# Kernel tuning notes

Hardware: AMD Instinct MI355X
Metric: run time of the kernel (lower is better)

## Reference

```python
import jax, jax.numpy as jnp
import numpy as np

SCALE = 4.0  # InputEmbedding scale


def setup_inputs() -> dict:
    key = jax.random.key(0)
    ks = jax.random.split(key, 16)
    T_obs, T_pred, N, E, H = 9, 12, 16384, 64, 128
    n_scenes = 512  # N / 32 tracks per scene
    inp = {
        "observed": jax.random.normal(ks[0], (T_obs, N, 2), jnp.float32),
        "prediction": jax.random.normal(ks[1], (T_pred, N, 2), jnp.float32),
        "goals": jax.random.normal(ks[2], (N, 2), jnp.float32),
        "batch_split": jnp.arange(0, N + 1, N // n_scenes, dtype=jnp.int64),
        # InputEmbedding: Linear(2 -> E)
        "W_emb": jax.random.normal(ks[3], (E, 2), jnp.float32) * 0.5,
        "b_emb": jax.random.normal(ks[4], (E,), jnp.float32) * 0.1,
        # LSTMCell(E -> H)
        "W_ih": jax.random.normal(ks[5], (4 * H, E), jnp.float32) * 0.08,
        "W_hh": jax.random.normal(ks[6], (4 * H, H), jnp.float32) * 0.08,
        "b_ih": jax.random.normal(ks[7], (4 * H,), jnp.float32) * 0.05,
        "b_hh": jax.random.normal(ks[8], (4 * H,), jnp.float32) * 0.05,
        # real_classifier MLP: [H, H/2, H/4, 1], ReLU after every Linear
        "W1": jax.random.normal(ks[9], (H // 2, H), jnp.float32) * 0.08,
        "b1": jnp.zeros((H // 2,), jnp.float32),
        "W2": jax.random.normal(ks[10], (H // 4, H // 2), jnp.float32) * 0.12,
        "b2": jnp.zeros((H // 4,), jnp.float32),
        "W3": jax.random.normal(ks[11], (1, H // 4), jnp.float32) * 0.2,
        "b3": jnp.zeros((1,), jnp.float32),
    }
    return inp


def _lstm_cell(x, h, c, W_ih, W_hh, b_ih, b_hh):
    gates = x @ W_ih.T + b_ih + h @ W_hh.T + b_hh  # [N, 4H]
    i, f, g, o = jnp.split(gates, 4, axis=-1)
    i = jax.nn.sigmoid(i)
    f = jax.nn.sigmoid(f)
    o = jax.nn.sigmoid(o)
    g = jnp.tanh(g)
    c2 = f * c + i * g
    h2 = o * jnp.tanh(c2)
    return h2, c2


def reference(observed, prediction, goals, batch_split,
              W_emb, b_emb, W_ih, W_hh, b_ih, b_hh,
              W1, b1, W2, b2, W3, b3):
    # pool=None, goal_flag=False -> step is: NaN-mask, velocity embed, LSTMCell,
    # masked write-back of (h, c) for valid tracks only.
    obs = jnp.concatenate([observed, prediction], axis=0)  # [T, N, 2]
    N = obs.shape[1]
    H = W_hh.shape[1]

    def step(carry, o12):
        h, c = carry
        o1, o2 = o12
        mask = ~(jnp.isnan(o1[:, 0]) | jnp.isnan(o2[:, 0]))  # [N]
        vel = jnp.where(mask[:, None], o2 - o1, 0.0)  # [N, 2]
        emb = (vel * SCALE) @ W_emb.T + b_emb  # [N, E]
        h2, c2 = _lstm_cell(emb, h, c, W_ih, W_hh, b_ih, b_hh)
        h = jnp.where(mask[:, None], h2, h)
        c = jnp.where(mask[:, None], c2, c)
        return (h, c), None

    h0 = jnp.zeros((N, H), obs.dtype)
    c0 = jnp.zeros((N, H), obs.dtype)
    (h, _c), _ = jax.lax.scan(step, (h0, c0), (obs[:-1], obs[1:]))

    primary = h[batch_split[:-1]]  # [batch_size, H]
    # make_mlp with relu appends ReLU after every Linear, including the last.
    x = jax.nn.relu(primary @ W1.T + b1)
    x = jax.nn.relu(x @ W2.T + b2)
    scores = jax.nn.relu(x @ W3.T + b3)  # [batch_size, 1]
    return scores
```

## Files before the change

### kernel.cpp

```cpp
#include <hip/hip_runtime.h>
#include <math.h>

#define SCALE 4.0f
#define H 128
#define E 64
#define NS 2
#define TMAX 32

#define WS_UC_OFF  131072

typedef _Float16 f16x8 __attribute__((ext_vector_type(8)));
typedef __attribute__((ext_vector_type(4))) float f32x4;

__device__ __forceinline__ bool is_nanf(float x) {
    return (__float_as_uint(x) & 0x7fffffffu) > 0x7f800000u;
}
__device__ __forceinline__ float rcpf(float x) { return __builtin_amdgcn_rcpf(x); }
__device__ __forceinline__ float sigm(float x) { return rcpf(1.0f + __expf(-x)); }
__device__ __forceinline__ float tanhfast(float x) {
    return fmaf(2.0f, rcpf(1.0f + __expf(-2.0f * x)), -1.0f);
}

__global__ __launch_bounds__(256)
void prep_kernel(const float* __restrict__ W_hh,
                 const float* __restrict__ W_ih,
                 const float* __restrict__ W_emb,
                 const float* __restrict__ b_emb,
                 const float* __restrict__ b_ih,
                 const float* __restrict__ b_hh,
                 char* __restrict__ ws)
{
    const int gid = blockIdx.x * 256 + threadIdx.x;
    if (gid < 8192) {
        const int lane = gid & 63;
        const int kb   = (gid >> 6) & 3;
        const int q    = (gid >> 8) & 3;
        const int w8   = gid >> 10;
        const int mt   = q * 8 + w8;
        const int row  = mt * 16 + (lane & 15);
        const int col0 = kb * 32 + (lane >> 4) * 8;
        const float* p = W_hh + (size_t)row * H + col0;
        f16x8 h8;
        #pragma unroll
        for (int j = 0; j < 8; ++j) h8[j] = (_Float16)p[j];
        *(f16x8*)(ws + (size_t)gid * 16) = h8;
    } else if (gid < 8192 + 512) {
        const int r = gid - 8192;
        const float* wr = W_ih + (size_t)r * E;
        float s0 = 0.f, s1 = 0.f, sc = 0.f;
        #pragma unroll 8
        for (int k = 0; k < E; ++k) {
            const float wv = wr[k];
            s0 += wv * W_emb[2 * k + 0];
            s1 += wv * W_emb[2 * k + 1];
            sc += wv * b_emb[k];
        }
        f32x4 v = {s0, s1, sc + b_ih[r] + b_hh[r], 0.0f};
        *(f32x4*)(ws + WS_UC_OFF + (size_t)r * 16) = v;
    }
}

__global__ __launch_bounds__(512, 2)
void lstm_disc_kernel(
    const float* __restrict__ observed,
    const float* __restrict__ prediction,
    const int* __restrict__ batch_split,
    const char* __restrict__ ws,
    const float* __restrict__ W1, const float* __restrict__ b1,
    const float* __restrict__ W2, const float* __restrict__ b2,
    const float* __restrict__ W3, const float* __restrict__ b3,
    float* __restrict__ out,
    int N, int T_obs, int T_total, int n_scenes)
{
    __shared__ __align__(16) _Float16 hT[2][4][NS][32];
    __shared__ float h32[NS][H];
    __shared__ float px[NS][TMAX], py[NS][TMAX];
    __shared__ float aA[NS][TMAX], bA[NS][TMAX];
    __shared__ int   mA[NS][TMAX];
    __shared__ float x1s[NS][H / 2];
    __shared__ float x2s[NS][H / 4];

    const int tid  = threadIdx.x;
    const int wave = tid >> 6;
    const int lane = tid & 63;
    const int ln15 = lane & 15;
    const int g4   = lane >> 4;
    const int esc  = ln15 & 1;
    const int ea   = (ln15 >> 1) & 3;
    const int rep  = ln15 >> 3;
    const int eu   = wave * 16 + g4 * 4 + ea;
    const int sc0  = blockIdx.x * NS;

    f16x8 afr[4][4];
    #pragma unroll
    for (int q = 0; q < 4; ++q)
        #pragma unroll
        for (int kb = 0; kb < 4; ++kb) {
            const size_t slot = ((size_t)((wave * 4 + q) * 4 + kb) * 64 + lane) * 16;
            afr[q][kb] = *(const f16x8*)(ws + slot);
        }

    float U0r[4], U1r[4], Ccr[4];
    #pragma unroll
    for (int q = 0; q < 4; ++q) {
        const f32x4 v = *(const f32x4*)(ws + WS_UC_OFF + (size_t)(eu + q * H) * 16);
        U0r[q] = v[0]; U1r[q] = v[1]; Ccr[q] = v[2];
    }

    if (tid < NS * TMAX) {
        const int s = tid >> 5, t = tid & 31;
        const int scene = sc0 + s;
        const int agent = (scene < n_scenes) ? batch_split[scene] : 0;
        if (t < T_total) {
            const float* src = (t < T_obs)
                ? (observed   + (size_t)t           * N * 2)
                : (prediction + (size_t)(t - T_obs) * N * 2);
            px[s][t] = src[(size_t)agent * 2 + 0];
            py[s][t] = src[(size_t)agent * 2 + 1];
        }
    }
    if (tid < 256) ((int*)hT)[tid] = 0;
    __syncthreads();

    if (tid < NS * TMAX) {
        const int s = tid >> 5, t = tid & 31;
        if (t < T_total - 1) {
            const bool m = !(is_nanf(px[s][t]) || is_nanf(px[s][t + 1]));
            aA[s][t] = m ? SCALE * (px[s][t + 1] - px[s][t]) : 0.0f;
            bA[s][t] = m ? SCALE * (py[s][t + 1] - py[s][t]) : 0.0f;
            mA[s][t] = m ? 1 : 0;
        }
    }

    const int wb_kb = eu >> 5;
    const int wb_k  = eu & 31;

    float c_st = 0.f, h_st = 0.f;
    __syncthreads();

    for (int t = 0; t < T_total - 1; ++t) {
        const int rp = t & 1, wp = rp ^ 1;

        const float aa = aA[esc][t];
        const float bb = bA[esc][t];
        const int   mm = mA[esc][t];

        f16x8 bf[4];
        #pragma unroll
        for (int kb = 0; kb < 4; ++kb)
            bf[kb] = *(const f16x8*)&hT[rp][kb][esc][g4 * 8];

        f32x4 acc[4];
        #pragma unroll
        for (int q = 0; q < 4; ++q) acc[q] = (f32x4){0.f, 0.f, 0.f, 0.f};
        #pragma unroll
        for (int kb = 0; kb < 4; ++kb)
            #pragma unroll
            for (int q = 0; q < 4; ++q)
                acc[q] = __builtin_amdgcn_mfma_f32_16x16x32_f16(afr[q][kb], bf[kb], acc[q], 0, 0, 0);

        const float p0 = acc[0][ea] + Ccr[0] + aa * U0r[0] + bb * U1r[0];
        const float p1 = acc[1][ea] + Ccr[1] + aa * U0r[1] + bb * U1r[1];
        const float p2 = acc[2][ea] + Ccr[2] + aa * U0r[2] + bb * U1r[2];
        const float p3 = acc[3][ea] + Ccr[3] + aa * U0r[3] + bb * U1r[3];
        const float ig = sigm(p0);
        const float fg = sigm(p1);
        const float gg = tanhfast(p2);
        const float og = sigm(p3);
        const float c2 = fg * c_st + ig * gg;
        const float h2 = og * tanhfast(c2);
        if (mm) { c_st = c2; h_st = h2; }

        if (rep == 0) {
            hT[wp][wb_kb][esc][wb_k] = (_Float16)h_st;
            if (t == T_total - 2) h32[esc][eu] = h_st;
        }
        __syncthreads();
    }

    if (tid < NS * (H / 2)) {
        const int s = tid >> 6, u = tid & 63;
        const float4* wr = (const float4*)(W1 + (size_t)u * H);
        const float4* hv = (const float4*)h32[s];
        float sum = b1[u];
        #pragma unroll
        for (int k = 0; k < H / 4; ++k) {
            const float4 w = wr[k], h = hv[k];
            sum += h.x * w.x + h.y * w.y + h.z * w.z + h.w * w.w;
        }
        x1s[s][u] = fmaxf(sum, 0.f);
    }
    __syncthreads();
    if (tid < NS * (H / 4)) {
        const int s = tid >> 5, u = tid & 31;
        const float4* wr = (const float4*)(W2 + (size_t)u * (H / 2));
        const float4* xv = (const float4*)x1s[s];
        float sum = b2[u];
        #pragma unroll
        for (int k = 0; k < H / 8; ++k) {
            const float4 w = wr[k], x = xv[k];
            sum += x.x * w.x + x.y * w.y + x.z * w.z + x.w * w.w;
        }
        x2s[s][u] = fmaxf(sum, 0.f);
    }
    __syncthreads();
    if (tid < NS) {
        const int scene = sc0 + tid;
        if (scene < n_scenes) {
            float sum = b3[0];
            #pragma unroll
            for (int k = 0; k < H / 4; ++k) sum += x2s[tid][k] * W3[k];
            out[scene] = fmaxf(sum, 0.f);
        }
    }
}

extern "C" void kernel_launch(void* const* d_in, const int* in_sizes, int n_in,
                              void* d_out, int out_size, void* d_ws, size_t ws_size,
                              hipStream_t stream) {
    const float* observed   = (const float*)d_in[0];
    const float* prediction = (const float*)d_in[1];
    const int*   batch_split = (const int*)d_in[3];
    const float* W_emb = (const float*)d_in[4];
    const float* b_emb = (const float*)d_in[5];
    const float* W_ih  = (const float*)d_in[6];
    const float* W_hh  = (const float*)d_in[7];
    const float* b_ih  = (const float*)d_in[8];
    const float* b_hh  = (const float*)d_in[9];
    const float* W1 = (const float*)d_in[10];
    const float* b1 = (const float*)d_in[11];
    const float* W2 = (const float*)d_in[12];
    const float* b2 = (const float*)d_in[13];
    const float* W3 = (const float*)d_in[14];
    const float* b3 = (const float*)d_in[15];
    float* out = (float*)d_out;

    const int N       = in_sizes[2] / 2;
    const int T_obs   = in_sizes[0] / (2 * N);
    const int T_total = T_obs + in_sizes[1] / (2 * N);
    const int n_scenes = in_sizes[3] - 1;

    prep_kernel<<<34, 256, 0, stream>>>(
        W_hh, W_ih, W_emb, b_emb, b_ih, b_hh, (char*)d_ws);

    const int nblocks = (n_scenes + NS - 1) / NS;
    lstm_disc_kernel<<<nblocks, 512, 0, stream>>>(
        observed, prediction, batch_split, (const char*)d_ws,
        W1, b1, W2, b2, W3, b3,
        out, N, T_obs, T_total, n_scenes);
}
```

Measured before the change: 105.9 us.

## Process one scene per block and raise occupancy bound to four blocks per CU

Each 512-thread block now runs the LSTM recurrence for a single scene instead of two, so the grid doubles to n_scenes blocks. Launch bounds move from 2 to 4 blocks per CU to let more blocks be resident. The MFMA B-operand columns are now replicated across the 16 lanes instead of holding two scenes, so each block does the same matrix work for half the useful output. The aim is to spread the latency-bound serial recurrence over more CUs and overlap more blocks, at the cost of more weight-fragment loads and register pressure under the tighter bound.

```diff
diff --git a/kernel.cpp b/kernel.cpp
--- a/kernel.cpp
+++ b/kernel.cpp
@@ -4,7 +4,6 @@
 #define SCALE 4.0f
 #define H 128
 #define E 64
-#define NS 2
 #define TMAX 32
 
 #define WS_UC_OFF  131072
@@ -60,7 +59,7 @@
     }
 }
 
-__global__ __launch_bounds__(512, 2)
+__global__ __launch_bounds__(512, 4)
 void lstm_disc_kernel(
     const float* __restrict__ observed,
     const float* __restrict__ prediction,
@@ -72,24 +71,23 @@
     float* __restrict__ out,
     int N, int T_obs, int T_total, int n_scenes)
 {
-    __shared__ __align__(16) _Float16 hT[2][4][NS][32];
-    __shared__ float h32[NS][H];
-    __shared__ float px[NS][TMAX], py[NS][TMAX];
-    __shared__ float aA[NS][TMAX], bA[NS][TMAX];
-    __shared__ int   mA[NS][TMAX];
-    __shared__ float x1s[NS][H / 2];
-    __shared__ float x2s[NS][H / 4];
+    __shared__ __align__(16) _Float16 hT[2][4][32];
+    __shared__ float h32[H];
+    __shared__ float px[TMAX], py[TMAX];
+    __shared__ float aA[TMAX], bA[TMAX];
+    __shared__ int   mA[TMAX];
+    __shared__ float x1s[H / 2];
+    __shared__ float x2s[H / 4];
 
     const int tid  = threadIdx.x;
     const int wave = tid >> 6;
     const int lane = tid & 63;
     const int ln15 = lane & 15;
     const int g4   = lane >> 4;
-    const int esc  = ln15 & 1;
-    const int ea   = (ln15 >> 1) & 3;
-    const int rep  = ln15 >> 3;
+    const int ea   = ln15 & 3;
+    const int rep  = ln15 >> 2;
     const int eu   = wave * 16 + g4 * 4 + ea;
-    const int sc0  = blockIdx.x * NS;
+    const int scene = blockIdx.x;
 
     f16x8 afr[4][4];
     #pragma unroll
@@ -107,29 +105,24 @@
         U0r[q] = v[0]; U1r[q] = v[1]; Ccr[q] = v[2];
     }
 
-    if (tid < NS * TMAX) {
-        const int s = tid >> 5, t = tid & 31;
-        const int scene = sc0 + s;
+    if (tid < TMAX && tid < T_total) {
+        const int t = tid;
         const int agent = (scene < n_scenes) ? batch_split[scene] : 0;
-        if (t < T_total) {
-            const float* src = (t < T_obs)
-                ? (observed   + (size_t)t           * N * 2)
-                : (prediction + (size_t)(t - T_obs) * N * 2);
-            px[s][t] = src[(size_t)agent * 2 + 0];
-            py[s][t] = src[(size_t)agent * 2 + 1];
-        }
-    }
-    if (tid < 256) ((int*)hT)[tid] = 0;
-    __syncthreads();
-
-    if (tid < NS * TMAX) {
-        const int s = tid >> 5, t = tid & 31;
-        if (t < T_total - 1) {
-            const bool m = !(is_nanf(px[s][t]) || is_nanf(px[s][t + 1]));
-            aA[s][t] = m ? SCALE * (px[s][t + 1] - px[s][t]) : 0.0f;
-            bA[s][t] = m ? SCALE * (py[s][t + 1] - py[s][t]) : 0.0f;
-            mA[s][t] = m ? 1 : 0;
-        }
+        const float* src = (t < T_obs)
+            ? (observed   + (size_t)t           * N * 2)
+            : (prediction + (size_t)(t - T_obs) * N * 2);
+        px[t] = src[(size_t)agent * 2 + 0];
+        py[t] = src[(size_t)agent * 2 + 1];
+    }
+    if (tid < 128) ((int*)hT)[tid] = 0;
+    __syncthreads();
+
+    if (tid < T_total - 1) {
+        const int t = tid;
+        const bool m = !(is_nanf(px[t]) || is_nanf(px[t + 1]));
+        aA[t] = m ? SCALE * (px[t + 1] - px[t]) : 0.0f;
+        bA[t] = m ? SCALE * (py[t + 1] - py[t]) : 0.0f;
+        mA[t] = m ? 1 : 0;
     }
 
     const int wb_kb = eu >> 5;
@@ -141,14 +134,14 @@
     for (int t = 0; t < T_total - 1; ++t) {
         const int rp = t & 1, wp = rp ^ 1;
 
-        const float aa = aA[esc][t];
-        const float bb = bA[esc][t];
-        const int   mm = mA[esc][t];
+        const float aa = aA[t];
+        const float bb = bA[t];
+        const int   mm = mA[t];
 
         f16x8 bf[4];
         #pragma unroll
         for (int kb = 0; kb < 4; ++kb)
-            bf[kb] = *(const f16x8*)&hT[rp][kb][esc][g4 * 8];
+            bf[kb] = *(const f16x8*)&hT[rp][kb][g4 * 8];
 
         f32x4 acc[4];
         #pragma unroll
@@ -172,46 +165,41 @@
         if (mm) { c_st = c2; h_st = h2; }
 
         if (rep == 0) {
-            hT[wp][wb_kb][esc][wb_k] = (_Float16)h_st;
-            if (t == T_total - 2) h32[esc][eu] = h_st;
+            hT[wp][wb_kb][wb_k] = (_Float16)h_st;
+            if (t == T_total - 2) h32[eu] = h_st;
         }
         __syncthreads();
     }
 
-    if (tid < NS * (H / 2)) {
-        const int s = tid >> 6, u = tid & 63;
-        const float4* wr = (const float4*)(W1 + (size_t)u * H);
-        const float4* hv = (const float4*)h32[s];
-        float sum = b1[u];
+    if (tid < H / 2) {
+        const float4* wr = (const float4*)(W1 + (size_t)tid * H);
+        const float4* hv = (const float4*)h32;
+        float sum = b1[tid];
         #pragma unroll
         for (int k = 0; k < H / 4; ++k) {
             const float4 w = wr[k], h = hv[k];
             sum += h.x * w.x + h.y * w.y + h.z * w.z + h.w * w.w;
         }
-        x1s[s][u] = fmaxf(sum, 0.f);
-    }
-    __syncthreads();
-    if (tid < NS * (H / 4)) {
-        const int s = tid >> 5, u = tid & 31;
-        const float4* wr = (const float4*)(W2 + (size_t)u * (H / 2));
-        const float4* xv = (const float4*)x1s[s];
-        float sum = b2[u];
+        x1s[tid] = fmaxf(sum, 0.f);
+    }
+    __syncthreads();
+    if (tid < H / 4) {
+        const float4* wr = (const float4*)(W2 + (size_t)tid * (H / 2));
+        const float4* xv = (const float4*)x1s;
+        float sum = b2[tid];
         #pragma unroll
         for (int k = 0; k < H / 8; ++k) {
             const float4 w = wr[k], x = xv[k];
             sum += x.x * w.x + x.y * w.y + x.z * w.z + x.w * w.w;
         }
-        x2s[s][u] = fmaxf(sum, 0.f);
-    }
-    __syncthreads();
-    if (tid < NS) {
-        const int scene = sc0 + tid;
-        if (scene < n_scenes) {
-            float sum = b3[0];
-            #pragma unroll
-            for (int k = 0; k < H / 4; ++k) sum += x2s[tid][k] * W3[k];
-            out[scene] = fmaxf(sum, 0.f);
-        }
+        x2s[tid] = fmaxf(sum, 0.f);
+    }
+    __syncthreads();
+    if (tid == 0 && scene < n_scenes) {
+        float sum = b3[0];
+        #pragma unroll
+        for (int k = 0; k < H / 4; ++k) sum += x2s[k] * W3[k];
+        out[scene] = fmaxf(sum, 0.f);
     }
 }
 
@@ -243,8 +231,7 @@
     prep_kernel<<<34, 256, 0, stream>>>(
         W_hh, W_ih, W_emb, b_emb, b_ih, b_hh, (char*)d_ws);
 
-    const int nblocks = (n_scenes + NS - 1) / NS;
-    lstm_disc_kernel<<<nblocks, 512, 0, stream>>>(
+    lstm_disc_kernel<<<n_scenes, 512, 0, stream>>>(
         observed, prediction, batch_split, (const char*)d_ws,
         W1, b1, W2, b2, W3, b3,
         out, N, T_obs, T_total, n_scenes);
```

After: 110.9 us. 4.7% more time.
